# Kernel tuning notes

Measured on AMD Instinct MI355X. Metric: run time of the kernel, lower is better.

## Reference

```python
import jax, jax.numpy as jnp
import numpy as np

N_HEADS = 32
N_KV_HEADS = 8


def _rope(x, cos, sin):
    # x: [B, S, H, D]; cos/sin: [S, D//2]; complex multiply on consecutive pairs
    B, S, H, D = x.shape
    xr = x.reshape(B, S, H, D // 2, 2)
    x0, x1 = xr[..., 0], xr[..., 1]
    c = cos[None, :, None, :]
    s = sin[None, :, None, :]
    o0 = x0 * c - x1 * s
    o1 = x0 * s + x1 * c
    return jnp.stack([o0, o1], axis=-1).reshape(B, S, H, D)


def setup_inputs():
    key = jax.random.key(0)
    ks = jax.random.split(key, 5)
    B, S, D = 1, 2048, 2048
    hd = D // N_HEADS  # 64
    x = jax.random.normal(ks[0], (B, S, D), jnp.float32)
    wq = jax.random.normal(ks[1], (D, D), jnp.float32) * 0.02
    wk = jax.random.normal(ks[2], (D, N_KV_HEADS * hd), jnp.float32) * 0.02
    wv = jax.random.normal(ks[3], (D, N_KV_HEADS * hd), jnp.float32) * 0.02
    wo = jax.random.normal(ks[4], (D, D), jnp.float32) * 0.02
    # true rotary frequencies (theta_cis = exp(i * pos * freq)), shape [S, hd//2]
    pos = jnp.arange(S, dtype=jnp.float32)
    freqs = 1.0 / (10000.0 ** (jnp.arange(0, hd, 2, dtype=jnp.float32) / hd))
    ang = pos[:, None] * freqs[None, :]
    return {"x": x, "theta_cos": jnp.cos(ang), "theta_sin": jnp.sin(ang),
            "wq": wq, "wk": wk, "wv": wv, "wo": wo}


def reference(x, theta_cos, theta_sin, wq, wk, wv, wo):
    B, S, D = x.shape
    hd = D // N_HEADS
    rep = N_HEADS // N_KV_HEADS
    xq = (x @ wq).reshape(B, S, N_HEADS, hd)
    # NOTE: module applies RoPE to K and V (not Q) - reproduced faithfully
    xk = _rope((x @ wk).reshape(B, S, N_KV_HEADS, hd), theta_cos, theta_sin)
    xv = _rope((x @ wv).reshape(B, S, N_KV_HEADS, hd), theta_cos, theta_sin)
    # GQA: repeat_interleave kv heads along head dim
    xk = jnp.repeat(xk, rep, axis=2)
    xv = jnp.repeat(xv, rep, axis=2)
    att = jnp.einsum('bqhd,bkhd->bhqk', xq, xk) * (hd ** -0.5)
    # faithful to torch.tril + masked_fill(att == 0.0, -inf)
    att = jnp.tril(att)
    att = jnp.where(att == 0.0, -jnp.inf, att)
    att = jax.nn.softmax(att, axis=-1)
    y = jnp.einsum('bhqk,bkhd->bqhd', att, xv).reshape(B, S, D)
    return y @ wo
```

## Files before the change

### kernel.cpp

```cpp
#include <hip/hip_runtime.h>

typedef unsigned short u16;
typedef unsigned int   u32;
typedef __bf16 bf16x8 __attribute__((ext_vector_type(8)));
typedef float  f32x4  __attribute__((ext_vector_type(4)));

__device__ __forceinline__ u16 f2bf(float f) {
    u32 x = __builtin_bit_cast(u32, f);
    x += 0x7fffu + ((x >> 16) & 1u);
    return (u16)(x >> 16);
}

__device__ __forceinline__ bf16x8 ld_frag(const u16* p) {
    return __builtin_bit_cast(bf16x8, *(const uint4*)p);
}

__device__ __forceinline__ f32x4 mfma16(bf16x8 a, bf16x8 b, f32x4 c) {
    return __builtin_amdgcn_mfma_f32_16x16x32_bf16(a, b, c, 0, 0, 0);
}

__device__ __forceinline__ void gl_lds16(const u16* g, u16* l) {
#if __has_builtin(__builtin_amdgcn_global_load_lds)
    __builtin_amdgcn_global_load_lds(
        (__attribute__((address_space(1))) const void*)g,
        (__attribute__((address_space(3))) void*)l, 16, 0, 0);
#else
    *(uint4*)l = *(const uint4*)g;
#endif
}

__global__ void f2b_vec(const float* __restrict__ in, u16* __restrict__ out, int n4) {
    int i = blockIdx.x * blockDim.x + threadIdx.x;
    if (i >= n4) return;
    float4 v = ((const float4*)in)[i];
    u32 a = (u32)f2bf(v.x) | ((u32)f2bf(v.y) << 16);
    u32 b = (u32)f2bf(v.z) | ((u32)f2bf(v.w) << 16);
    ((uint2*)out)[i] = make_uint2(a, b);
}

__global__ void transpose_f2b(const float* __restrict__ in, u16* __restrict__ out, int R, int C) {
    __shared__ float t[32][33];
    int c0 = blockIdx.x * 32, r0 = blockIdx.y * 32;
    for (int i = threadIdx.y; i < 32; i += 8)
        t[i][threadIdx.x] = in[(size_t)(r0 + i) * C + c0 + threadIdx.x];
    __syncthreads();
    for (int i = threadIdx.y; i < 32; i += 8)
        out[(size_t)(c0 + i) * R + r0 + threadIdx.x] = f2bf(t[threadIdx.x][i]);
}

__device__ __forceinline__ void gemm_core(const u16* __restrict__ A, const u16* __restrict__ BT,
                                          float* Cf, u16* Cb, int m0, int n0, int N, int Kstride,
                                          int ks, int ke) {
    __shared__ __align__(16) u16 As[128 * 32];
    __shared__ __align__(16) u16 Bs[128 * 32];
    const int tid = threadIdx.x, wave = tid >> 6, lane = tid & 63;
    const int quad = lane >> 4, l15 = lane & 15;
    const int wr = wave >> 1, wc = wave & 1;
    f32x4 acc[4][4] = {};
    for (int k0 = ks; k0 < ke; k0 += 32) {
        const u16* Ag = A + (size_t)m0 * Kstride + k0;
        const u16* Bg = BT + (size_t)n0 * Kstride + k0;
#pragma unroll
        for (int r2 = 0; r2 < 2; r2++) {
            int i = r2 * 256 + tid;
            gl_lds16(Ag + (size_t)(i >> 2) * Kstride + (i & 3) * 8, &As[i * 8]);
            gl_lds16(Bg + (size_t)(i >> 2) * Kstride + (i & 3) * 8, &Bs[i * 8]);
        }
        __syncthreads();
        bf16x8 af[4], bfr[4];
#pragma unroll
        for (int i = 0; i < 4; i++) {
            af[i]  = ld_frag(&As[(wr * 64 + i * 16 + l15) * 32 + quad * 8]);
            bfr[i] = ld_frag(&Bs[(wc * 64 + i * 16 + l15) * 32 + quad * 8]);
        }
#pragma unroll
        for (int i = 0; i < 4; i++)
#pragma unroll
            for (int j = 0; j < 4; j++)
                acc[i][j] = mfma16(af[i], bfr[j], acc[i][j]);
        __syncthreads();
    }
    if (Cb) {
#pragma unroll
        for (int i = 0; i < 4; i++)
#pragma unroll
            for (int r = 0; r < 4; r++) {
                u16* p = Cb + (size_t)(m0 + wr * 64 + i * 16 + quad * 4 + r) * N + n0 + wc * 64 + l15;
#pragma unroll
                for (int j = 0; j < 4; j++) p[j * 16] = f2bf(acc[i][j][r]);
            }
    } else {
#pragma unroll
        for (int i = 0; i < 4; i++)
#pragma unroll
            for (int r = 0; r < 4; r++) {
                float* p = Cf + (size_t)(m0 + wr * 64 + i * 16 + quad * 4 + r) * N + n0 + wc * 64 + l15;
#pragma unroll
                for (int j = 0; j < 4; j++) p[j * 16] = acc[i][j][r];
            }
    }
}

__global__ __launch_bounds__(256) void gemm_proj(const u16* __restrict__ A,
                                                 const u16* __restrict__ wqT,
                                                 const u16* __restrict__ wkT,
                                                 const u16* __restrict__ wvT,
                                                 u16* Qb, float* Kraw, float* Vraw) {
    int bx = blockIdx.x, m0 = blockIdx.y * 128;
    if (bx < 16)      gemm_core(A, wqT, nullptr, Qb, m0, bx * 128, 2048, 2048, 0, 2048);
    else if (bx < 20) gemm_core(A, wkT, Kraw, nullptr, m0, (bx - 16) * 128, 512, 2048, 0, 2048);
    else              gemm_core(A, wvT, Vraw, nullptr, m0, (bx - 20) * 128, 512, 2048, 0, 2048);
}

__global__ __launch_bounds__(256) void gemm_out_split(const u16* __restrict__ A,
                                                      const u16* __restrict__ BT,
                                                      float* __restrict__ Cpart) {
    int z = blockIdx.z;
    gemm_core(A, BT, Cpart + (size_t)z * 2048 * 2048, nullptr,
              blockIdx.y * 128, blockIdx.x * 128, 2048, 2048, z * 1024, (z + 1) * 1024);
}

__global__ void combine_out(const float* __restrict__ Cpart, float* __restrict__ out) {
    int i = blockIdx.x * 256 + threadIdx.x;
    float4 a = ((const float4*)Cpart)[i];
    float4 b = ((const float4*)(Cpart + 2048 * 2048))[i];
    float4 o; o.x = a.x + b.x; o.y = a.y + b.y; o.z = a.z + b.z; o.w = a.w + b.w;
    ((float4*)out)[i] = o;
}

__global__ void rope_kernel(const float* __restrict__ Kraw, float* __restrict__ Vraw,
                            const float* __restrict__ cosb, const float* __restrict__ sinb,
                            u16* __restrict__ Kb) {
    int p = blockIdx.x * 256 + threadIdx.x;
    int s = p >> 8, rem = p & 255, t = rem & 31;
    float c = cosb[s * 32 + t], sn = sinb[s * 32 + t];
    float2 k2 = ((const float2*)Kraw)[p];
    float k0 = k2.x * c - k2.y * sn, k1 = k2.x * sn + k2.y * c;
    ((u32*)Kb)[p] = (u32)f2bf(k0) | ((u32)f2bf(k1) << 16);
    float2 v2 = ((const float2*)Vraw)[p];
    float2 o;
    o.x = v2.x * c - v2.y * sn;
    o.y = v2.x * sn + v2.y * c;
    ((float2*)Vraw)[p] = o;
}

#define LPK 72
#define LPV 136
#define T_(q,l,h) (((u32)(q) << 16) | ((u32)(l) << 8) | (u32)(h))
__device__ const u32 ATASK[48] = {
    T_(14,0,15), T_(15,0,16), T_(28,0,16), T_(29,0,16), T_(30,0,16), T_(31,0,16), T_(30,16,31), T_(31,16,32),
    T_(12,0,13), T_(13,0,14), T_(24,0,14), T_(25,0,14), T_(26,0,14), T_(27,0,14), T_(26,14,27), T_(27,14,28),
    T_(28,16,29), T_(29,16,30),
    T_(10,0,11), T_(11,0,12), T_(20,0,12), T_(21,0,12), T_(22,0,12), T_(23,0,12), T_(22,12,23), T_(23,12,24),
    T_(24,14,25), T_(25,14,26),
    T_(8,0,9), T_(9,0,10), T_(16,0,10), T_(17,0,10), T_(18,0,10), T_(19,0,10), T_(18,10,19), T_(19,10,20),
    T_(20,12,21), T_(21,12,22),
    T_(6,0,7), T_(7,0,8), T_(16,10,17), T_(17,10,18),
    T_(4,0,5), T_(5,0,6), T_(2,0,3), T_(3,0,4), T_(0,0,1), T_(1,0,2)
};

struct AttnSmem {
    u16 Ks[128 * LPK];
    u16 Vs[64 * LPV];
    u16 QPs[4 * 16 * LPV];
};

__global__ __launch_bounds__(256) void attn_kernel(const u16* __restrict__ Qb,
                                                   const u16* __restrict__ Kb,
                                                   const u16* __restrict__ VbT,
                                                   u16* __restrict__ Yb,
                                                   float* __restrict__ Opart,
                                                   float* __restrict__ lpart) {
    __shared__ __align__(16) AttnSmem sm;
    const int tid = threadIdx.x, w = tid >> 6, lane = tid & 63;
    const int quad = lane >> 4, l15 = lane & 15;
    const int h = blockIdx.x, kvh = h >> 2;
    const u32 tk = ATASK[blockIdx.y];
    const int qt = tk >> 16, lo = (tk >> 8) & 255, hi = tk & 255;
    const bool partial = (qt >= 16);
    const int pt = partial ? ((qt - 16) * 2 + (lo != 0)) : 0;
    const int q0 = qt * 64;

    const u16* Qg = Qb + (size_t)q0 * 2048 + h * 64;
#pragma unroll
    for (int r2 = 0; r2 < 2; r2++) {
        int i = r2 * 256 + tid, row = i >> 3, c8 = (i & 7) * 8;
        *(uint4*)&sm.QPs[row * LPK + c8] = *(const uint4*)(Qg + (size_t)row * 2048 + c8);
    }
    __syncthreads();
    bf16x8 aQ0 = ld_frag(&sm.QPs[(w * 16 + l15) * LPK + quad * 8]);
    bf16x8 aQ1 = ld_frag(&sm.QPs[(w * 16 + l15) * LPK + 32 + quad * 8]);

    f32x4 O[4] = {};
    float l_acc[4] = {0.f, 0.f, 0.f, 0.f};
    u16* Ps = &sm.QPs[w * 16 * LPV];
    const int qrow = q0 + w * 16 + quad * 4;

    for (int jt = lo; jt < hi; jt += 2) {
        const int j0 = jt * 64;
        __syncthreads();
        const u16* Kg = Kb + (size_t)j0 * 512 + kvh * 64;
        const u16* Vg = VbT + (size_t)(kvh * 64) * 2048 + j0;
#pragma unroll
        for (int r2 = 0; r2 < 4; r2++) {
            int i = r2 * 256 + tid;
            int krow = i >> 3, kc = (i & 7) * 8;
            *(uint4*)&sm.Ks[krow * LPK + kc] = *(const uint4*)(Kg + (size_t)krow * 512 + kc);
            int vrow = i >> 4, vc = (i & 15) * 8;
            *(uint4*)&sm.Vs[vrow * LPV + vc] = *(const uint4*)(Vg + (size_t)vrow * 2048 + vc);
        }
        __syncthreads();

        f32x4 s[8];
#pragma unroll
        for (int j = 0; j < 8; j++) {
            bf16x8 b0 = ld_frag(&sm.Ks[(j * 16 + l15) * LPK + quad * 8]);
            bf16x8 b1 = ld_frag(&sm.Ks[(j * 16 + l15) * LPK + 32 + quad * 8]);
            f32x4 z = {};
            z = mfma16(aQ0, b0, z);
            z = mfma16(aQ1, b1, z);
            s[j] = z;
        }
        const bool needmask = (jt + 1) >= qt;
#pragma unroll
        for (int j = 0; j < 8; j++)
#pragma unroll
            for (int r = 0; r < 4; r++) {
                float p = __expf(s[j][r] * 0.125f);
                if (needmask && (j0 + j * 16 + l15) > (qrow + r)) p = 0.f;
                s[j][r] = p;
                l_acc[r] += p;
            }
#pragma unroll
        for (int j = 0; j < 8; j++)
#pragma unroll
            for (int r = 0; r < 4; r++)
                Ps[(quad * 4 + r) * LPV + j * 16 + l15] = f2bf(s[j][r]);
        bf16x8 aP[4];
#pragma unroll
        for (int kk = 0; kk < 4; kk++)
            aP[kk] = ld_frag(&Ps[l15 * LPV + kk * 32 + quad * 8]);
#pragma unroll
        for (int j = 0; j < 4; j++)
#pragma unroll
            for (int kk = 0; kk < 4; kk++) {
                bf16x8 v = ld_frag(&sm.Vs[(j * 16 + l15) * LPV + kk * 32 + quad * 8]);
                O[j] = mfma16(aP[kk], v, O[j]);
            }
    }
    float l_i[4];
#pragma unroll
    for (int r = 0; r < 4; r++) {
        float rs = l_acc[r];
        rs += __shfl_xor(rs, 1); rs += __shfl_xor(rs, 2);
        rs += __shfl_xor(rs, 4); rs += __shfl_xor(rs, 8);
        l_i[r] = rs;
    }
    if (!partial) {
#pragma unroll
        for (int r = 0; r < 4; r++) {
            float inv = __frcp_rn(l_i[r]);
#pragma unroll
            for (int j = 0; j < 4; j++)
                Yb[(size_t)(q0 + w * 16 + quad * 4 + r) * 2048 + h * 64 + j * 16 + l15] =
                    f2bf(O[j][r] * inv);
        }
    } else {
        float* Og = Opart + ((size_t)(pt * 32 + h) * 64) * 64;
#pragma unroll
        for (int r = 0; r < 4; r++) {
            int row = w * 16 + quad * 4 + r;
#pragma unroll
            for (int j = 0; j < 4; j++)
                Og[(size_t)row * 64 + j * 16 + l15] = O[j][r];
            if (l15 == 0) lpart[(size_t)(pt * 32 + h) * 64 + row] = l_i[r];
        }
    }
}

__global__ void combine_kernel(const float* __restrict__ Opart,
                               const float* __restrict__ lpart,
                               u16* __restrict__ Yb) {
    int e = blockIdx.x * 256 + threadIdx.x;
    int d4 = e & 15, h = (e >> 4) & 31, rg = e >> 9;
    int t16 = rg >> 6, row = rg & 63;
    int s0 = (t16 * 2) * 32 + h, s1 = s0 + 32;
    float4 a = ((const float4*)Opart)[((size_t)s0 * 64 + row) * 16 + d4];
    float4 b = ((const float4*)Opart)[((size_t)s1 * 64 + row) * 16 + d4];
    float l = lpart[(size_t)s0 * 64 + row] + lpart[(size_t)s1 * 64 + row];
    float inv = __frcp_rn(l);
    u32 lo = (u32)f2bf((a.x + b.x) * inv) | ((u32)f2bf((a.y + b.y) * inv) << 16);
    u32 hi = (u32)f2bf((a.z + b.z) * inv) | ((u32)f2bf((a.w + b.w) * inv) << 16);
    int q = 1024 + rg;
    ((uint2*)(Yb + (size_t)q * 2048 + h * 64))[d4] = make_uint2(lo, hi);
}

extern "C" void kernel_launch(void* const* d_in, const int* in_sizes, int n_in,
                              void* d_out, int out_size, void* d_ws, size_t ws_size,
                              hipStream_t stream) {
    const float* x  = (const float*)d_in[0];
    const float* tc = (const float*)d_in[1];
    const float* ts = (const float*)d_in[2];
    const float* wq = (const float*)d_in[3];
    const float* wk = (const float*)d_in[4];
    const float* wv = (const float*)d_in[5];
    const float* wo = (const float*)d_in[6];
    float* out = (float*)d_out;

    char* w = (char*)d_ws;
    u16*   xb   = (u16*)(w);
    u16*   Yb   = (u16*)(w);
    u16*   woT  = (u16*)(w + (8u  << 20));
    u16*   wkT  = (u16*)(w + (16u << 20));
    u16*   wvT  = (u16*)(w + (18u << 20));
    u16*   wqT  = (u16*)(w + (20u << 20));
    float* Kraw = (float*)(w + (28u << 20));
    float* Vraw = (float*)(w + (32u << 20));
    u16*   Kb   = (u16*)(w + (36u << 20));
    u16*   VbT  = (u16*)(w + (38u << 20));
    u16*   Qb   = (u16*)(w + (40u << 20));
    float* Opart= (float*)(w + (16u << 20));
    float* lpart= (float*)(w + (32u << 20));
    float* Cpart= (float*)(w + (16u << 20));

    f2b_vec<<<4096, 256, 0, stream>>>(x, xb, 1048576);
    transpose_f2b<<<dim3(64, 64), dim3(32, 8), 0, stream>>>(wq, wqT, 2048, 2048);
    transpose_f2b<<<dim3(16, 64), dim3(32, 8), 0, stream>>>(wk, wkT, 2048, 512);
    transpose_f2b<<<dim3(16, 64), dim3(32, 8), 0, stream>>>(wv, wvT, 2048, 512);
    transpose_f2b<<<dim3(64, 64), dim3(32, 8), 0, stream>>>(wo, woT, 2048, 2048);
    gemm_proj<<<dim3(24, 16), 256, 0, stream>>>(xb, wqT, wkT, wvT, Qb, Kraw, Vraw);
    rope_kernel<<<2048, 256, 0, stream>>>(Kraw, Vraw, tc, ts, Kb);
    transpose_f2b<<<dim3(16, 64), dim3(32, 8), 0, stream>>>(Vraw, VbT, 2048, 512);
    attn_kernel<<<dim3(32, 48), 256, 0, stream>>>(Qb, Kb, VbT, Yb, Opart, lpart);
    combine_kernel<<<2048, 256, 0, stream>>>(Opart, lpart, Yb);
    gemm_out_split<<<dim3(16, 16, 2), 256, 0, stream>>>(Yb, woT, Cpart);
    combine_out<<<4096, 256, 0, stream>>>(Cpart, out);
}
```

Measured before the change: 280.0 us.

## Fuse prep kernels, split-K projections with bf16 partials, prefetch KV in attention

```diff
diff --git a/kernel.cpp b/kernel.cpp
--- a/kernel.cpp
+++ b/kernel.cpp
@@ -10,6 +10,8 @@
     x += 0x7fffu + ((x >> 16) & 1u);
     return (u16)(x >> 16);
 }
+__device__ __forceinline__ float bflo(u32 u) { return __builtin_bit_cast(float, u << 16); }
+__device__ __forceinline__ float bfhi(u32 u) { return __builtin_bit_cast(float, u & 0xffff0000u); }
 
 __device__ __forceinline__ bf16x8 ld_frag(const u16* p) {
     return __builtin_bit_cast(bf16x8, *(const uint4*)p);
@@ -29,27 +31,43 @@
 #endif
 }
 
-__global__ void f2b_vec(const float* __restrict__ in, u16* __restrict__ out, int n4) {
-    int i = blockIdx.x * blockDim.x + threadIdx.x;
-    if (i >= n4) return;
-    float4 v = ((const float4*)in)[i];
-    u32 a = (u32)f2bf(v.x) | ((u32)f2bf(v.y) << 16);
-    u32 b = (u32)f2bf(v.z) | ((u32)f2bf(v.w) << 16);
-    ((uint2*)out)[i] = make_uint2(a, b);
-}
-
-__global__ void transpose_f2b(const float* __restrict__ in, u16* __restrict__ out, int R, int C) {
+__device__ __forceinline__ void tr_f2b(const float* __restrict__ in, u16* __restrict__ out,
+                                       int R, int C, int c0, int r0, float (*t)[33], int tid) {
+    int tx = tid & 31, ty = tid >> 5;
+    for (int i = ty; i < 32; i += 8)
+        t[i][tx] = in[(size_t)(r0 + i) * C + c0 + tx];
+    __syncthreads();
+    for (int i = ty; i < 32; i += 8)
+        out[(size_t)(c0 + i) * R + r0 + tx] = f2bf(t[tx][i]);
+}
+
+__global__ __launch_bounds__(256) void prep(const float* __restrict__ x,
+                                            const float* __restrict__ wq,
+                                            const float* __restrict__ wk,
+                                            const float* __restrict__ wv,
+                                            u16* xb, u16* wqT, u16* wkT, u16* wvT) {
     __shared__ float t[32][33];
-    int c0 = blockIdx.x * 32, r0 = blockIdx.y * 32;
-    for (int i = threadIdx.y; i < 32; i += 8)
-        t[i][threadIdx.x] = in[(size_t)(r0 + i) * C + c0 + threadIdx.x];
-    __syncthreads();
-    for (int i = threadIdx.y; i < 32; i += 8)
-        out[(size_t)(c0 + i) * R + r0 + threadIdx.x] = f2bf(t[threadIdx.x][i]);
+    int bx = blockIdx.x, tid = threadIdx.x;
+    if (bx < 4096) {
+        int i = bx * 256 + tid;
+        float4 v = ((const float4*)x)[i];
+        u32 a = (u32)f2bf(v.x) | ((u32)f2bf(v.y) << 16);
+        u32 b = (u32)f2bf(v.z) | ((u32)f2bf(v.w) << 16);
+        ((uint2*)xb)[i] = make_uint2(a, b);
+    } else if (bx < 8192) {
+        int b = bx - 4096;
+        tr_f2b(wq, wqT, 2048, 2048, (b & 63) * 32, (b >> 6) * 32, t, tid);
+    } else if (bx < 9216) {
+        int b = bx - 8192;
+        tr_f2b(wk, wkT, 2048, 512, (b & 15) * 32, (b >> 4) * 32, t, tid);
+    } else {
+        int b = bx - 9216;
+        tr_f2b(wv, wvT, 2048, 512, (b & 15) * 32, (b >> 4) * 32, t, tid);
+    }
 }
 
 __device__ __forceinline__ void gemm_core(const u16* __restrict__ A, const u16* __restrict__ BT,
-                                          float* Cf, u16* Cb, int m0, int n0, int N, int Kstride,
+                                          u16* Cb, int m0, int n0, int N, int Kstride,
                                           int ks, int ke) {
     __shared__ __align__(16) u16 As[128 * 32];
     __shared__ __align__(16) u16 Bs[128 * 32];
@@ -80,68 +98,74 @@
                 acc[i][j] = mfma16(af[i], bfr[j], acc[i][j]);
         __syncthreads();
     }
-    if (Cb) {
-#pragma unroll
-        for (int i = 0; i < 4; i++)
-#pragma unroll
-            for (int r = 0; r < 4; r++) {
-                u16* p = Cb + (size_t)(m0 + wr * 64 + i * 16 + quad * 4 + r) * N + n0 + wc * 64 + l15;
-#pragma unroll
-                for (int j = 0; j < 4; j++) p[j * 16] = f2bf(acc[i][j][r]);
-            }
-    } else {
-#pragma unroll
-        for (int i = 0; i < 4; i++)
-#pragma unroll
-            for (int r = 0; r < 4; r++) {
-                float* p = Cf + (size_t)(m0 + wr * 64 + i * 16 + quad * 4 + r) * N + n0 + wc * 64 + l15;
-#pragma unroll
-                for (int j = 0; j < 4; j++) p[j * 16] = acc[i][j][r];
-            }
-    }
+#pragma unroll
+    for (int i = 0; i < 4; i++)
+#pragma unroll
+        for (int r = 0; r < 4; r++) {
+            u16* p = Cb + (size_t)(m0 + wr * 64 + i * 16 + quad * 4 + r) * N + n0 + wc * 64 + l15;
+#pragma unroll
+            for (int j = 0; j < 4; j++) p[j * 16] = f2bf(acc[i][j][r]);
+        }
 }
 
 __global__ __launch_bounds__(256) void gemm_proj(const u16* __restrict__ A,
                                                  const u16* __restrict__ wqT,
                                                  const u16* __restrict__ wkT,
                                                  const u16* __restrict__ wvT,
-                                                 u16* Qb, float* Kraw, float* Vraw) {
-    int bx = blockIdx.x, m0 = blockIdx.y * 128;
-    if (bx < 16)      gemm_core(A, wqT, nullptr, Qb, m0, bx * 128, 2048, 2048, 0, 2048);
-    else if (bx < 20) gemm_core(A, wkT, Kraw, nullptr, m0, (bx - 16) * 128, 512, 2048, 0, 2048);
-    else              gemm_core(A, wvT, Vraw, nullptr, m0, (bx - 20) * 128, 512, 2048, 0, 2048);
-}
-
-__global__ __launch_bounds__(256) void gemm_out_split(const u16* __restrict__ A,
-                                                      const u16* __restrict__ BT,
-                                                      float* __restrict__ Cpart) {
-    int z = blockIdx.z;
-    gemm_core(A, BT, Cpart + (size_t)z * 2048 * 2048, nullptr,
-              blockIdx.y * 128, blockIdx.x * 128, 2048, 2048, z * 1024, (z + 1) * 1024);
-}
-
-__global__ void combine_out(const float* __restrict__ Cpart, float* __restrict__ out) {
-    int i = blockIdx.x * 256 + threadIdx.x;
-    float4 a = ((const float4*)Cpart)[i];
-    float4 b = ((const float4*)(Cpart + 2048 * 2048))[i];
-    float4 o; o.x = a.x + b.x; o.y = a.y + b.y; o.z = a.z + b.z; o.w = a.w + b.w;
-    ((float4*)out)[i] = o;
-}
-
-__global__ void rope_kernel(const float* __restrict__ Kraw, float* __restrict__ Vraw,
-                            const float* __restrict__ cosb, const float* __restrict__ sinb,
-                            u16* __restrict__ Kb) {
-    int p = blockIdx.x * 256 + threadIdx.x;
-    int s = p >> 8, rem = p & 255, t = rem & 31;
-    float c = cosb[s * 32 + t], sn = sinb[s * 32 + t];
-    float2 k2 = ((const float2*)Kraw)[p];
-    float k0 = k2.x * c - k2.y * sn, k1 = k2.x * sn + k2.y * c;
-    ((u32*)Kb)[p] = (u32)f2bf(k0) | ((u32)f2bf(k1) << 16);
-    float2 v2 = ((const float2*)Vraw)[p];
-    float2 o;
-    o.x = v2.x * c - v2.y * sn;
-    o.y = v2.x * sn + v2.y * c;
-    ((float2*)Vraw)[p] = o;
+                                                 u16* Qp, u16* Kp, u16* Vp) {
+    int bx = blockIdx.x, m0 = blockIdx.y * 128, z = blockIdx.z;
+    int ks = z * 1024, ke = ks + 1024;
+    if (bx < 16)      gemm_core(A, wqT, Qp + (size_t)z * 4194304, m0, bx * 128, 2048, 2048, ks, ke);
+    else if (bx < 20) gemm_core(A, wkT, Kp + (size_t)z * 1048576, m0, (bx - 16) * 128, 512, 2048, ks, ke);
+    else              gemm_core(A, wvT, Vp + (size_t)z * 1048576, m0, (bx - 20) * 128, 512, 2048, ks, ke);
+}
+
+__global__ __launch_bounds__(256) void rope_combine(const u16* __restrict__ Qp,
+                                                    const u16* __restrict__ Kp,
+                                                    const u16* __restrict__ Vp,
+                                                    const float* __restrict__ tc,
+                                                    const float* __restrict__ tsn,
+                                                    const float* __restrict__ wo,
+                                                    u16* Qb, u16* Kb, u16* Vb, u16* woT) {
+    __shared__ float t[32][33];
+    int bx = blockIdx.x, tid = threadIdx.x;
+    if (bx < 4096) {
+        int i = bx * 256 + tid;
+        uint2 a = ((const uint2*)Qp)[i];
+        uint2 b = ((const uint2*)(Qp + 4194304))[i];
+        u32 r0_ = (u32)f2bf(bflo(a.x) + bflo(b.x)) | ((u32)f2bf(bfhi(a.x) + bfhi(b.x)) << 16);
+        u32 r1_ = (u32)f2bf(bflo(a.y) + bflo(b.y)) | ((u32)f2bf(bfhi(a.y) + bfhi(b.y)) << 16);
+        ((uint2*)Qb)[i] = make_uint2(r0_, r1_);
+    } else if (bx < 6144) {
+        int s = bx - 4096, pr = tid, tt = pr & 31;
+        float c = tc[s * 32 + tt], sn = tsn[s * 32 + tt];
+        u32 a = ((const u32*)Kp)[s * 256 + pr];
+        u32 b = ((const u32*)(Kp + 1048576))[s * 256 + pr];
+        float e = bflo(a) + bflo(b), o = bfhi(a) + bfhi(b);
+        ((u32*)Kb)[s * 256 + pr] = (u32)f2bf(e * c - o * sn) | ((u32)f2bf(e * sn + o * c) << 16);
+    } else if (bx < 8192) {
+        int s = bx - 6144, pr = tid, tt = pr & 31;
+        float c = tc[s * 32 + tt], sn = tsn[s * 32 + tt];
+        u32 a = ((const u32*)Vp)[s * 256 + pr];
+        u32 b = ((const u32*)(Vp + 1048576))[s * 256 + pr];
+        float e = bflo(a) + bflo(b), o = bfhi(a) + bfhi(b);
+        ((u32*)Vb)[s * 256 + pr] = (u32)f2bf(e * c - o * sn) | ((u32)f2bf(e * sn + o * c) << 16);
+    } else {
+        int b = bx - 8192;
+        tr_f2b(wo, woT, 2048, 2048, (b & 63) * 32, (b >> 6) * 32, t, tid);
+    }
+}
+
+__global__ __launch_bounds__(256) void transpose_b2b(const u16* __restrict__ in,
+                                                     u16* __restrict__ out) {
+    __shared__ u16 t[32][33];
+    int tid = threadIdx.x, tx = tid & 31, ty = tid >> 5;
+    int c0 = blockIdx.x * 32, r0 = blockIdx.y * 32;
+    for (int i = ty; i < 32; i += 8)
+        t[i][tx] = in[(size_t)(r0 + i) * 512 + c0 + tx];
+    __syncthreads();
+    for (int i = ty; i < 32; i += 8)
+        out[(size_t)(c0 + i) * 2048 + r0 + tx] = t[tx][i];
 }
 
 #define LPK 72
@@ -196,20 +220,41 @@
     u16* Ps = &sm.QPs[w * 16 * LPV];
     const int qrow = q0 + w * 16 + quad * 4;
 
+    const u16* Kg0 = Kb + kvh * 64;
+    const u16* Vg0 = VbT + (size_t)(kvh * 64) * 2048;
+
+    uint4 kv[8];
+    {
+        const u16* Kg = Kg0 + (size_t)(lo * 64) * 512;
+        const u16* Vg = Vg0 + lo * 64;
+#pragma unroll
+        for (int r2 = 0; r2 < 4; r2++) {
+            int i = r2 * 256 + tid;
+            kv[r2]     = *(const uint4*)(Kg + (size_t)(i >> 3) * 512 + (i & 7) * 8);
+            kv[4 + r2] = *(const uint4*)(Vg + (size_t)(i >> 4) * 2048 + (i & 15) * 8);
+        }
+    }
+
     for (int jt = lo; jt < hi; jt += 2) {
         const int j0 = jt * 64;
         __syncthreads();
-        const u16* Kg = Kb + (size_t)j0 * 512 + kvh * 64;
-        const u16* Vg = VbT + (size_t)(kvh * 64) * 2048 + j0;
 #pragma unroll
         for (int r2 = 0; r2 < 4; r2++) {
             int i = r2 * 256 + tid;
-            int krow = i >> 3, kc = (i & 7) * 8;
-            *(uint4*)&sm.Ks[krow * LPK + kc] = *(const uint4*)(Kg + (size_t)krow * 512 + kc);
-            int vrow = i >> 4, vc = (i & 15) * 8;
-            *(uint4*)&sm.Vs[vrow * LPV + vc] = *(const uint4*)(Vg + (size_t)vrow * 2048 + vc);
+            *(uint4*)&sm.Ks[(i >> 3) * LPK + (i & 7) * 8] = kv[r2];
+            *(uint4*)&sm.Vs[(i >> 4) * LPV + (i & 15) * 8] = kv[4 + r2];
         }
         __syncthreads();
+        if (jt + 2 < hi) {
+            const u16* Kg = Kg0 + (size_t)((jt + 2) * 64) * 512;
+            const u16* Vg = Vg0 + (jt + 2) * 64;
+#pragma unroll
+            for (int r2 = 0; r2 < 4; r2++) {
+                int i = r2 * 256 + tid;
+                kv[r2]     = *(const uint4*)(Kg + (size_t)(i >> 3) * 512 + (i & 7) * 8);
+                kv[4 + r2] = *(const uint4*)(Vg + (size_t)(i >> 4) * 2048 + (i & 15) * 8);
+            }
+        }
 
         f32x4 s[8];
 #pragma unroll
@@ -221,16 +266,24 @@
             z = mfma16(aQ1, b1, z);
             s[j] = z;
         }
-        const bool needmask = (jt + 1) >= qt;
-#pragma unroll
-        for (int j = 0; j < 8; j++)
-#pragma unroll
-            for (int r = 0; r < 4; r++) {
-                float p = __expf(s[j][r] * 0.125f);
-                if (needmask && (j0 + j * 16 + l15) > (qrow + r)) p = 0.f;
-                s[j][r] = p;
-                l_acc[r] += p;
-            }
+        if (jt + 1 >= qt) {
+#pragma unroll
+            for (int j = 0; j < 8; j++)
+#pragma unroll
+                for (int r = 0; r < 4; r++) {
+                    float p = __expf(s[j][r] * 0.125f);
+                    if ((j0 + j * 16 + l15) > (qrow + r)) p = 0.f;
+                    s[j][r] = p; l_acc[r] += p;
+                }
+        } else {
+#pragma unroll
+            for (int j = 0; j < 8; j++)
+#pragma unroll
+                for (int r = 0; r < 4; r++) {
+                    float p = __expf(s[j][r] * 0.125f);
+                    s[j][r] = p; l_acc[r] += p;
+                }
+        }
 #pragma unroll
         for (int j = 0; j < 8; j++)
 #pragma unroll
@@ -295,6 +348,28 @@
     ((uint2*)(Yb + (size_t)q * 2048 + h * 64))[d4] = make_uint2(lo, hi);
 }
 
+__global__ __launch_bounds__(256) void gemm_out_split(const u16* __restrict__ A,
+                                                      const u16* __restrict__ BT,
+                                                      u16* C0, u16* C1, u16* C2, u16* C3) {
+    int z = blockIdx.z;
+    u16* dst = z == 0 ? C0 : z == 1 ? C1 : z == 2 ? C2 : C3;
+    gemm_core(A, BT, dst, blockIdx.y * 128, blockIdx.x * 128, 2048, 2048, z * 512, (z + 1) * 512);
+}
+
+__global__ void combine_out(const u16* __restrict__ C0, const u16* __restrict__ C1,
+                            const u16* __restrict__ C2, const u16* __restrict__ C3,
+                            float* __restrict__ out) {
+    int i = blockIdx.x * 256 + threadIdx.x;
+    uint2 a = ((const uint2*)C0)[i], b = ((const uint2*)C1)[i];
+    uint2 c = ((const uint2*)C2)[i], d = ((const uint2*)C3)[i];
+    float4 o;
+    o.x = bflo(a.x) + bflo(b.x) + bflo(c.x) + bflo(d.x);
+    o.y = bfhi(a.x) + bfhi(b.x) + bfhi(c.x) + bfhi(d.x);
+    o.z = bflo(a.y) + bflo(b.y) + bflo(c.y) + bflo(d.y);
+    o.w = bfhi(a.y) + bfhi(b.y) + bfhi(c.y) + bfhi(d.y);
+    ((float4*)out)[i] = o;
+}
+
 extern "C" void kernel_launch(void* const* d_in, const int* in_sizes, int n_in,
                               void* d_out, int out_size, void* d_ws, size_t ws_size,
                               hipStream_t stream) {
@@ -309,30 +384,31 @@
 
     char* w = (char*)d_ws;
     u16*   xb   = (u16*)(w);
-    u16*   Yb   = (u16*)(w);
-    u16*   woT  = (u16*)(w + (8u  << 20));
+    u16*   wqT  = (u16*)(w + (8u  << 20));
     u16*   wkT  = (u16*)(w + (16u << 20));
     u16*   wvT  = (u16*)(w + (18u << 20));
-    u16*   wqT  = (u16*)(w + (20u << 20));
-    float* Kraw = (float*)(w + (28u << 20));
-    float* Vraw = (float*)(w + (32u << 20));
-    u16*   Kb   = (u16*)(w + (36u << 20));
-    u16*   VbT  = (u16*)(w + (38u << 20));
-    u16*   Qb   = (u16*)(w + (40u << 20));
-    float* Opart= (float*)(w + (16u << 20));
-    float* lpart= (float*)(w + (32u << 20));
-    float* Cpart= (float*)(w + (16u << 20));
-
-    f2b_vec<<<4096, 256, 0, stream>>>(x, xb, 1048576);
-    transpose_f2b<<<dim3(64, 64), dim3(32, 8), 0, stream>>>(wq, wqT, 2048, 2048);
-    transpose_f2b<<<dim3(16, 64), dim3(32, 8), 0, stream>>>(wk, wkT, 2048, 512);
-    transpose_f2b<<<dim3(16, 64), dim3(32, 8), 0, stream>>>(wv, wvT, 2048, 512);
-    transpose_f2b<<<dim3(64, 64), dim3(32, 8), 0, stream>>>(wo, woT, 2048, 2048);
-    gemm_proj<<<dim3(24, 16), 256, 0, stream>>>(xb, wqT, wkT, wvT, Qb, Kraw, Vraw);
-    rope_kernel<<<2048, 256, 0, stream>>>(Kraw, Vraw, tc, ts, Kb);
-    transpose_f2b<<<dim3(16, 64), dim3(32, 8), 0, stream>>>(Vraw, VbT, 2048, 512);
+    u16*   Qp   = (u16*)(w + (20u << 20));
+    u16*   Kp   = (u16*)(w + (36u << 20));
+    u16*   Vp   = (u16*)(w + (40u << 20));
+    u16*   Qb   = (u16*)(w);
+    u16*   woT  = (u16*)(w + (8u  << 20));
+    u16*   Kb   = (u16*)(w + (16u << 20));
+    u16*   Vb   = (u16*)(w + (18u << 20));
+    u16*   VbT  = (u16*)(w + (20u << 20));
+    float* lpart= (float*)(w + (22u << 20));
+    u16*   Yb   = (u16*)(w + (24u << 20));
+    float* Opart= (float*)(w + (32u << 20));
+    u16*   C0   = (u16*)(w);
+    u16*   C1   = (u16*)(w + (16u << 20));
+    u16*   C2   = (u16*)(w + (32u << 20));
+    u16*   C3   = (u16*)(w + (40u << 20));
+
+    prep<<<10240, 256, 0, stream>>>(x, wq, wk, wv, xb, wqT, wkT, wvT);
+    gemm_proj<<<dim3(24, 16, 2), 256, 0, stream>>>(xb, wqT, wkT, wvT, Qp, Kp, Vp);
+    rope_combine<<<12288, 256, 0, stream>>>(Qp, Kp, Vp, tc, ts, wo, Qb, Kb, Vb, woT);
+    transpose_b2b<<<dim3(16, 64), 256, 0, stream>>>(Vb, VbT);
     attn_kernel<<<dim3(32, 48), 256, 0, stream>>>(Qb, Kb, VbT, Yb, Opart, lpart);
     combine_kernel<<<2048, 256, 0, stream>>>(Opart, lpart, Yb);
-    gemm_out_split<<<dim3(16, 16, 2), 256, 0, stream>>>(Yb, woT, Cpart);
-    combine_out<<<4096, 256, 0, stream>>>(Cpart, out);
-}
+    gemm_out_split<<<dim3(16, 16, 4), 256, 0, stream>>>(Yb, woT, C0, C1, C2, C3);
+    combine_out<<<4096, 256, 0, stream>>>(C0, C1, C2, C3, out);
+}
```

Result: slower. 303.5 us (+8.4%).
